# Kernel tuning notes

Measured on AMD Instinct MI355X. Metric: run time of the kernel, lower is better.

The kernel has to match this reference:

```python
import jax, jax.numpy as jnp
import numpy as np

N_HEAD = 16
ROPE_BASE = 10000.0


def _rope_tables(T, head_dim, dtype):
    inv_freq = 1.0 / (ROPE_BASE ** (jnp.arange(0, head_dim, 2, dtype=jnp.float32) / head_dim))
    t = jnp.arange(T, dtype=jnp.float32)
    freqs = t[:, None] * inv_freq[None, :]          # [T, hd/2]
    emb = jnp.concatenate([freqs, freqs], axis=-1)  # [T, hd]
    return jnp.cos(emb).astype(dtype), jnp.sin(emb).astype(dtype)


def _rotate_half(x):
    h = x.shape[-1] // 2
    return jnp.concatenate([-x[..., h:], x[..., :h]], axis=-1)


def setup_inputs() -> dict:
    key = jax.random.key(0)
    k1, k2, k3 = jax.random.split(key, 3)
    B, T, C = 2, 2048, 1024
    x = jax.random.normal(k1, (B, T, C), dtype=jnp.float32)
    w_attn = jax.random.normal(k2, (3 * C, C), dtype=jnp.float32) * (1.0 / np.sqrt(C))
    w_proj = jax.random.normal(k3, (C, C), dtype=jnp.float32) * (1.0 / np.sqrt(C))
    return {"x": x, "w_attn": w_attn, "w_proj": w_proj}


def reference(x, w_attn, w_proj):
    B, T, C = x.shape
    H = N_HEAD
    hd = C // H

    qkv = jnp.einsum('btc,fc->btf', x, w_attn)          # [B,T,3C]
    q, k, v = jnp.split(qkv, 3, axis=-1)
    # [B,H,T,hd]
    q = q.reshape(B, T, H, hd).transpose(0, 2, 1, 3)
    k = k.reshape(B, T, H, hd).transpose(0, 2, 1, 3)
    v = v.reshape(B, T, H, hd).transpose(0, 2, 1, 3)

    cos, sin = _rope_tables(T, hd, x.dtype)             # [T,hd]
    cos = cos[None, None]
    sin = sin[None, None]
    q = q * cos + _rotate_half(q) * sin
    k = k * cos + _rotate_half(k) * sin

    scale = 1.0 / np.sqrt(hd)
    scores = jnp.einsum('bhqd,bhkd->bhqk', q, k) * scale  # [B,H,T,T]
    causal = jnp.tril(jnp.ones((T, T), dtype=bool))
    scores = jnp.where(causal[None, None], scores, jnp.finfo(scores.dtype).min)
    attn = jax.nn.softmax(scores, axis=-1)
    out = jnp.einsum('bhqk,bhkd->bhqd', attn, v)          # [B,H,T,hd]
    out = out.transpose(0, 2, 1, 3).reshape(B, T, C)
    return jnp.einsum('btc,oc->bto', out, w_proj)
```

## Files before the change

kernel.cpp:

```cpp
#include <hip/hip_runtime.h>
#include <hip/hip_bf16.h>
#include <stdint.h>

typedef unsigned short u16;
typedef __bf16 bf16x8 __attribute__((ext_vector_type(8)));
typedef float f32x4 __attribute__((ext_vector_type(4)));

#define B_ 2
#define T_ 2048
#define C_ 1024
#define H_ 16
#define HD 64
#define M_ (B_ * T_)
#define N3 (3 * C_)

__device__ __forceinline__ float bf2f(u16 u) {
  return __uint_as_float(((unsigned int)u) << 16);
}
__device__ __forceinline__ u16 f2bf(float f) {
  unsigned int u = __float_as_uint(f);
  u += 0x7FFF + ((u >> 16) & 1);
  return (u16)(u >> 16);
}
__device__ __forceinline__ unsigned cvt_pk_bf16(float lo, float hi) {
  unsigned r;
  asm("v_cvt_pk_bf16_f32 %0, %1, %2" : "=v"(r) : "v"(lo), "v"(hi));
  return r;
}
__device__ __forceinline__ void async16(void* ldsp, const void* gp) {
  __builtin_amdgcn_global_load_lds(
      (const __attribute__((address_space(1))) unsigned int*)gp,
      (__attribute__((address_space(3))) unsigned int*)ldsp, 16, 0, 0);
}

union U16x8 { uint4 v; u16 u[8]; };

__device__ __forceinline__ bf16x8 ldsAfrag(const char* base, int row, int kbyte) {
  int off = (row * 128 + kbyte) ^ ((row & 7) << 4);
  uint4 t = *reinterpret_cast<const uint4*>(base + off);
  return __builtin_bit_cast(bf16x8, t);
}
__device__ __forceinline__ bf16x8 ldsRead(const char* p) {
  uint4 t = *reinterpret_cast<const uint4*>(p);
  return __builtin_bit_cast(bf16x8, t);
}

__global__ void cvt_bf16(const float* __restrict__ src, u16* __restrict__ dst, int n4) {
  int i = blockIdx.x * blockDim.x + threadIdx.x;
  int stride = gridDim.x * blockDim.x;
  for (; i < n4; i += stride) {
    float4 v = reinterpret_cast<const float4*>(src)[i];
    uint2 o;
    o.x = (unsigned)f2bf(v.x) | ((unsigned)f2bf(v.y) << 16);
    o.y = (unsigned)f2bf(v.z) | ((unsigned)f2bf(v.w) << 16);
    reinterpret_cast<uint2*>(dst)[i] = o;
  }
}

__global__ void rope_tables_kernel(float* __restrict__ cosT, float* __restrict__ sinT) {
  int t = blockIdx.x;
  int i = threadIdx.x;
  float inv = powf(10000.0f, -(float)i * (1.0f / 32.0f));
  float f = (float)t * inv;
  cosT[t * 32 + i] = cosf(f);
  sinT[t * 32 + i] = sinf(f);
}

template <bool OUT_F32>
__global__ __launch_bounds__(256) void gemm_bt(const u16* __restrict__ A,
                                               const u16* __restrict__ Bw,
                                               void* __restrict__ Cout,
                                               int M, int N, int K) {
  __shared__ uint4 ldsbuf[2048];
  char* As = (char*)ldsbuf;
  char* Bs = (char*)ldsbuf + 16384;
  const int tid = threadIdx.x;
  const int lane = tid & 63;
  const int wv = tid >> 6;
  const int wr = wv >> 1, wc = wv & 1;
  const int lrow = lane & 15, lgrp = lane >> 4;
  const long m0 = (long)blockIdx.x * 128, n0 = (long)blockIdx.y * 128;
  const int srow_l = lane >> 3;
  const int csrc = ((lane & 7) ^ (lane >> 3)) * 8;
  f32x4 acc[4][4] = {};
  for (int k0 = 0; k0 < K; k0 += 64) {
    __syncthreads();
#pragma unroll
    for (int p = 0; p < 4; ++p) {
      int seg = wv * 4 + p;
      int row = seg * 8 + srow_l;
      async16(As + seg * 1024, A + (size_t)(m0 + row) * K + k0 + csrc);
      async16(Bs + seg * 1024, Bw + (size_t)(n0 + row) * K + k0 + csrc);
    }
    __syncthreads();
#pragma unroll
    for (int ks = 0; ks < 2; ++ks) {
      bf16x8 af[4], bfr[4];
#pragma unroll
      for (int i = 0; i < 4; ++i) {
        af[i]  = ldsAfrag(As, wr * 64 + i * 16 + lrow, ks * 64 + lgrp * 16);
        bfr[i] = ldsAfrag(Bs, wc * 64 + i * 16 + lrow, ks * 64 + lgrp * 16);
      }
#pragma unroll
      for (int i = 0; i < 4; ++i)
#pragma unroll
        for (int j = 0; j < 4; ++j)
          acc[i][j] = __builtin_amdgcn_mfma_f32_16x16x32_bf16(af[i], bfr[j], acc[i][j], 0, 0, 0);
    }
  }
#pragma unroll
  for (int i = 0; i < 4; ++i)
#pragma unroll
    for (int j = 0; j < 4; ++j) {
      long r0 = m0 + wr * 64 + i * 16 + lgrp * 4;
      long c  = n0 + wc * 64 + j * 16 + lrow;
#pragma unroll
      for (int r = 0; r < 4; ++r) {
        float v = acc[i][j][r];
        if (OUT_F32)
          ((float*)Cout)[(r0 + r) * N + c] = v;
        else
          ((u16*)Cout)[(r0 + r) * N + c] = f2bf(v);
      }
    }
}

__global__ __launch_bounds__(256) void rope_reshape(const u16* __restrict__ qkv,
                                                    const float* __restrict__ cosT,
                                                    const float* __restrict__ sinT,
                                                    u16* __restrict__ Q,
                                                    u16* __restrict__ K,
                                                    u16* __restrict__ Vt) {
  __shared__ u16 Vs[64][80];
  const float SCLQ = 0.125f * 1.4426950408889634f;
  const int tid = threadIdx.x;
  const int tblk = blockIdx.x, bh = blockIdx.y;
  const int b = bh >> 4, h = bh & 15;
  const int tl = tid >> 2, quar = tid & 3;
  const int t = tblk * 64 + tl;
  const u16* rowp = qkv + ((size_t)(b * T_ + t)) * N3 + h * HD;
  const int d0 = quar * 8;
  float cs[8], sn[8];
#pragma unroll
  for (int j = 0; j < 8; ++j) {
    cs[j] = cosT[t * 32 + d0 + j];
    sn[j] = sinT[t * 32 + d0 + j];
  }
#pragma unroll
  for (int part = 0; part < 2; ++part) {
    const u16* p = rowp + part * C_;
    U16x8 x1, x2, o1, o2;
    x1.v = *reinterpret_cast<const uint4*>(p + d0);
    x2.v = *reinterpret_cast<const uint4*>(p + d0 + 32);
#pragma unroll
    for (int j = 0; j < 8; ++j) {
      float a = bf2f(x1.u[j]), c2 = bf2f(x2.u[j]);
      float f1 = a * cs[j] - c2 * sn[j];
      float f2 = c2 * cs[j] + a * sn[j];
      if (part == 0) { f1 *= SCLQ; f2 *= SCLQ; }
      o1.u[j] = f2bf(f1);
      o2.u[j] = f2bf(f2);
    }
    u16* dst = (part ? K : Q) + ((size_t)bh * T_ + t) * HD;
    *reinterpret_cast<uint4*>(dst + d0) = o1.v;
    *reinterpret_cast<uint4*>(dst + d0 + 32) = o2.v;
  }
  const u16* pv = rowp + 2 * C_;
#pragma unroll
  for (int c = 0; c < 2; ++c) {
    int d = quar * 16 + c * 8;
    *reinterpret_cast<uint4*>(&Vs[tl][d]) = *reinterpret_cast<const uint4*>(pv + d);
  }
  __syncthreads();
  const int d = tid >> 2, tq = tid & 3;
  U16x8 a, bv;
#pragma unroll
  for (int j = 0; j < 8; ++j) a.u[j] = Vs[tq * 16 + j][d];
#pragma unroll
  for (int j = 0; j < 8; ++j) bv.u[j] = Vs[tq * 16 + 8 + j][d];
  u16* dstv = Vt + ((size_t)bh * HD + d) * T_ + tblk * 64 + tq * 16;
  *reinterpret_cast<uint4*>(dstv) = a.v;
  *reinterpret_cast<uint4*>(dstv + 8) = bv.v;
}

__global__ __launch_bounds__(256) void attn_fwd11(const u16* __restrict__ Q,
                                                  const u16* __restrict__ K,
                                                  const u16* __restrict__ Vt,
                                                  u16* __restrict__ O) {
  __shared__ uint4 lds4[2560];
  char* ldsb = (char*)lds4;
  const int tid = threadIdx.x;
  const int lane = tid & 63, wv = tid >> 6;
  const int lrow = lane & 15, lgrp = lane >> 4;
  const int bh = blockIdx.y;
  const int b = bh >> 4, h = bh & 15;
  const u16* Qh = Q + (size_t)bh * T_ * HD;
  const u16* Kh = K + (size_t)bh * T_ * HD;
  const u16* Vh = Vt + (size_t)bh * HD * T_;

  const int srow_l = lane >> 3;
  const int csrc = ((lane & 7) ^ (lane >> 3)) * 8;

  auto stage = [&](int slot, int kt) {
    char* Kd = ldsb + (slot << 14);
    char* Vd = Kd + 8192;
    const u16* Kg = Kh + (size_t)(kt * 64) * HD;
    const u16* Vg = Vh + kt * 64;
#pragma unroll
    for (int seg = 0; seg < 2; ++seg) {
      int row = wv * 16 + seg * 8 + srow_l;
      async16(Kd + wv * 2048 + seg * 1024, Kg + (size_t)row * HD + csrc);
      async16(Vd + wv * 2048 + seg * 1024, Vg + (size_t)row * T_ + csrc);
    }
  };

  const int swz = (lrow & 7) << 4;
  const int krA = lrow * 128 + ((lgrp * 16) ^ swz);
  const int krB = lrow * 128 + ((64 + lgrp * 16) ^ swz);
  const int vrA = 8192 + krA;
  const int vrB = 8192 + krB;
  char* PsW = ldsb + 32768 + wv * 2048 + lrow * 128;
  char* pw0 = PsW + ((0 * 32 + lgrp * 8) ^ swz);
  char* pw1 = PsW + ((1 * 32 + lgrp * 8) ^ swz);
  char* pw2 = PsW + ((2 * 32 + lgrp * 8) ^ swz);
  char* pw3 = PsW + ((3 * 32 + lgrp * 8) ^ swz);
  const char* paA = PsW + ((lgrp * 16) ^ swz);
  const char* paB = PsW + ((64 + lgrp * 16) ^ swz);

  uint4 ones4;
  ones4.x = ones4.y = ones4.z = ones4.w = 0x3F803F80u;
  const bf16x8 ones8 = __builtin_bit_cast(bf16x8, ones4);

  const int unit = 31 - (int)blockIdx.x;
  const int qs = unit * 64;
  const int q_glob = qs + wv * 16 + lrow;
  const int nu = unit + 1;

  bf16x8 qf[2];
#pragma unroll
  for (int ks = 0; ks < 2; ++ks) {
    uint4 t4 = *reinterpret_cast<const uint4*>(
        Qh + (size_t)(qs + wv * 16 + lrow) * HD + ks * 32 + lgrp * 8);
    qf[ks] = __builtin_bit_cast(bf16x8, t4);
  }
  f32x4 o[4] = {};
  f32x4 lacc = {};

  stage(0, 0);
  __syncthreads();

  int cur = 0;
  for (int kt = 0; kt < nu; ++kt) {
    if (kt + 1 < nu) stage(cur ^ 1, kt + 1);
    const char* buf = ldsb + (cur << 14);
    const char* KbA = buf + krA;
    const char* KbB = buf + krB;
    const char* VbA = buf + vrA;
    const char* VbB = buf + vrB;

    f32x4 s[4] = {};
    __builtin_amdgcn_s_setprio(1);
#pragma unroll
    for (int n = 0; n < 4; ++n)
      s[n] = __builtin_amdgcn_mfma_f32_16x16x32_bf16(ldsRead(KbA + n * 2048), qf[0], s[n], 0, 0, 0);
#pragma unroll
    for (int n = 0; n < 4; ++n)
      s[n] = __builtin_amdgcn_mfma_f32_16x16x32_bf16(ldsRead(KbB + n * 2048), qf[1], s[n], 0, 0, 0);
    __builtin_amdgcn_s_setprio(0);

    if (kt == nu - 1) {
#pragma unroll
      for (int n = 0; n < 4; ++n)
#pragma unroll
        for (int r = 0; r < 4; ++r) {
          int kg = kt * 64 + n * 16 + lgrp * 4 + r;
          float v = (kg <= q_glob) ? s[n][r] : -__builtin_inff();
          s[n][r] = exp2f(v);
        }
    } else {
#pragma unroll
      for (int n = 0; n < 4; ++n)
#pragma unroll
        for (int r = 0; r < 4; ++r) s[n][r] = exp2f(s[n][r]);
    }

    {
      uint2 w0, w1, w2, w3;
      w0.x = cvt_pk_bf16(s[0][0], s[0][1]); w0.y = cvt_pk_bf16(s[0][2], s[0][3]);
      w1.x = cvt_pk_bf16(s[1][0], s[1][1]); w1.y = cvt_pk_bf16(s[1][2], s[1][3]);
      w2.x = cvt_pk_bf16(s[2][0], s[2][1]); w2.y = cvt_pk_bf16(s[2][2], s[2][3]);
      w3.x = cvt_pk_bf16(s[3][0], s[3][1]); w3.y = cvt_pk_bf16(s[3][2], s[3][3]);
      *reinterpret_cast<uint2*>(pw0) = w0;
      *reinterpret_cast<uint2*>(pw1) = w1;
      *reinterpret_cast<uint2*>(pw2) = w2;
      *reinterpret_cast<uint2*>(pw3) = w3;
    }

    __builtin_amdgcn_s_setprio(1);
#pragma unroll
    for (int ks = 0; ks < 2; ++ks) {
      bf16x8 pa = ldsRead(ks ? paB : paA);
      lacc = __builtin_amdgcn_mfma_f32_16x16x32_bf16(pa, ones8, lacc, 0, 0, 0);
      const char* vbb = ks ? VbB : VbA;
#pragma unroll
      for (int dn = 0; dn < 4; ++dn) {
        bf16x8 bv = ldsRead(vbb + dn * 2048);
        o[dn] = __builtin_amdgcn_mfma_f32_16x16x32_bf16(pa, bv, o[dn], 0, 0, 0);
      }
    }
    __builtin_amdgcn_s_setprio(0);
    __syncthreads();
    cur ^= 1;
  }

#pragma unroll
  for (int r = 0; r < 4; ++r) {
    float inv = 1.0f / lacc[r];
    int t = qs + wv * 16 + lgrp * 4 + r;
#pragma unroll
    for (int dn = 0; dn < 4; ++dn) {
      int c = h * HD + dn * 16 + lrow;
      O[((size_t)(b * T_ + t)) * C_ + c] = f2bf(o[dn][r] * inv);
    }
  }
}

extern "C" void kernel_launch(void* const* d_in, const int* in_sizes, int n_in,
                              void* d_out, int out_size, void* d_ws, size_t ws_size,
                              hipStream_t stream) {
  const float* x  = (const float*)d_in[0];
  const float* wa = (const float*)d_in[1];
  const float* wp = (const float*)d_in[2];
  float* out = (float*)d_out;
  char* ws = (char*)d_ws;
  size_t off = 0;
  auto alloc = [&](size_t bytes) {
    char* p = ws + off;
    off += (bytes + 255) & ~(size_t)255;
    return p;
  };
  u16* xb   = (u16*)alloc((size_t)M_ * C_ * 2);
  u16* wab  = (u16*)alloc((size_t)N3 * C_ * 2);
  u16* wpb  = (u16*)alloc((size_t)C_ * C_ * 2);
  u16* qkvb = (u16*)alloc((size_t)M_ * N3 * 2);
  u16* Qb   = (u16*)alloc((size_t)B_ * H_ * T_ * HD * 2);
  u16* Kb   = (u16*)alloc((size_t)B_ * H_ * T_ * HD * 2);
  u16* Vtb  = (u16*)alloc((size_t)B_ * H_ * T_ * HD * 2);
  u16* Ob   = (u16*)alloc((size_t)M_ * C_ * 2);
  float* cosT = (float*)alloc((size_t)T_ * 32 * 4);
  float* sinT = (float*)alloc((size_t)T_ * 32 * 4);
  (void)in_sizes; (void)n_in; (void)out_size; (void)ws_size;

  cvt_bf16<<<1024, 256, 0, stream>>>(x, xb, M_ * C_ / 4);
  cvt_bf16<<<1024, 256, 0, stream>>>(wa, wab, N3 * C_ / 4);
  cvt_bf16<<<512, 256, 0, stream>>>(wp, wpb, C_ * C_ / 4);
  rope_tables_kernel<<<T_, 32, 0, stream>>>(cosT, sinT);
  gemm_bt<false><<<dim3(M_ / 128, N3 / 128), 256, 0, stream>>>(xb, wab, qkvb, M_, N3, C_);
  rope_reshape<<<dim3(T_ / 64, B_ * H_), 256, 0, stream>>>(qkvb, cosT, sinT, Qb, Kb, Vtb);
  attn_fwd11<<<dim3(32, B_ * H_), 256, 0, stream>>>(Qb, Kb, Vtb, Ob);
  gemm_bt<true><<<dim3(M_ / 128, C_ / 128), 256, 0, stream>>>(Ob, wpb, out, M_, C_, C_);
}
```

Baseline: 139.8 us.

## Process 128 query rows per attention block to reuse K/V tiles

The attention kernel now gives each wave two 16-row query tiles, so a block covers 128 queries instead of 64. Each K and V fragment read from LDS feeds two MFMAs, halving K/V staging traffic per query. The cost is a grid of 512 blocks instead of 1024, more registers per thread and a larger P buffer in LDS, which may lower occupancy. Because the grid is half as large, causal load imbalance across CUs is coarser.

```diff
diff --git a/kernel.cpp b/kernel.cpp
--- a/kernel.cpp
+++ b/kernel.cpp
@@ -183,11 +183,11 @@
   *reinterpret_cast<uint4*>(dstv + 8) = bv.v;
 }
 
-__global__ __launch_bounds__(256) void attn_fwd11(const u16* __restrict__ Q,
+__global__ __launch_bounds__(256) void attn_fwd12(const u16* __restrict__ Q,
                                                   const u16* __restrict__ K,
                                                   const u16* __restrict__ Vt,
                                                   u16* __restrict__ O) {
-  __shared__ uint4 lds4[2560];
+  __shared__ uint4 lds4[3072];
   char* ldsb = (char*)lds4;
   const int tid = threadIdx.x;
   const int lane = tid & 63, wv = tid >> 6;
@@ -219,7 +219,7 @@
   const int krB = lrow * 128 + ((64 + lgrp * 16) ^ swz);
   const int vrA = 8192 + krA;
   const int vrB = 8192 + krB;
-  char* PsW = ldsb + 32768 + wv * 2048 + lrow * 128;
+  char* PsW = ldsb + 32768 + wv * 4096 + lrow * 128;
   char* pw0 = PsW + ((0 * 32 + lgrp * 8) ^ swz);
   char* pw1 = PsW + ((1 * 32 + lgrp * 8) ^ swz);
   char* pw2 = PsW + ((2 * 32 + lgrp * 8) ^ swz);
@@ -231,20 +231,23 @@
   ones4.x = ones4.y = ones4.z = ones4.w = 0x3F803F80u;
   const bf16x8 ones8 = __builtin_bit_cast(bf16x8, ones4);
 
-  const int unit = 31 - (int)blockIdx.x;
-  const int qs = unit * 64;
-  const int q_glob = qs + wv * 16 + lrow;
-  const int nu = unit + 1;
-
-  bf16x8 qf[2];
-#pragma unroll
-  for (int ks = 0; ks < 2; ++ks) {
-    uint4 t4 = *reinterpret_cast<const uint4*>(
-        Qh + (size_t)(qs + wv * 16 + lrow) * HD + ks * 32 + lgrp * 8);
-    qf[ks] = __builtin_bit_cast(bf16x8, t4);
-  }
-  f32x4 o[4] = {};
-  f32x4 lacc = {};
+  const int unit = 15 - (int)blockIdx.x;
+  const int q0 = unit * 128;
+  const int qg0 = q0 + wv * 32 + lrow;
+  const int qg1 = qg0 + 16;
+  const int nu = unit * 2 + 2;
+
+  bf16x8 qf[2][2];
+#pragma unroll
+  for (int m = 0; m < 2; ++m)
+#pragma unroll
+    for (int ks = 0; ks < 2; ++ks) {
+      uint4 t4 = *reinterpret_cast<const uint4*>(
+          Qh + (size_t)(q0 + wv * 32 + m * 16 + lrow) * HD + ks * 32 + lgrp * 8);
+      qf[m][ks] = __builtin_bit_cast(bf16x8, t4);
+    }
+  f32x4 o[2][4] = {};
+  f32x4 lacc[2] = {};
 
   stage(0, 0);
   __syncthreads();
@@ -258,54 +261,68 @@
     const char* VbA = buf + vrA;
     const char* VbB = buf + vrB;
 
-    f32x4 s[4] = {};
+    f32x4 s[2][4] = {};
     __builtin_amdgcn_s_setprio(1);
 #pragma unroll
-    for (int n = 0; n < 4; ++n)
-      s[n] = __builtin_amdgcn_mfma_f32_16x16x32_bf16(ldsRead(KbA + n * 2048), qf[0], s[n], 0, 0, 0);
-#pragma unroll
-    for (int n = 0; n < 4; ++n)
-      s[n] = __builtin_amdgcn_mfma_f32_16x16x32_bf16(ldsRead(KbB + n * 2048), qf[1], s[n], 0, 0, 0);
+    for (int n = 0; n < 4; ++n) {
+      bf16x8 bk = ldsRead(KbA + n * 2048);
+      s[0][n] = __builtin_amdgcn_mfma_f32_16x16x32_bf16(bk, qf[0][0], s[0][n], 0, 0, 0);
+      s[1][n] = __builtin_amdgcn_mfma_f32_16x16x32_bf16(bk, qf[1][0], s[1][n], 0, 0, 0);
+    }
+#pragma unroll
+    for (int n = 0; n < 4; ++n) {
+      bf16x8 bk = ldsRead(KbB + n * 2048);
+      s[0][n] = __builtin_amdgcn_mfma_f32_16x16x32_bf16(bk, qf[0][1], s[0][n], 0, 0, 0);
+      s[1][n] = __builtin_amdgcn_mfma_f32_16x16x32_bf16(bk, qf[1][1], s[1][n], 0, 0, 0);
+    }
     __builtin_amdgcn_s_setprio(0);
 
-    if (kt == nu - 1) {
+    if (kt >= nu - 2) {
 #pragma unroll
       for (int n = 0; n < 4; ++n)
 #pragma unroll
         for (int r = 0; r < 4; ++r) {
           int kg = kt * 64 + n * 16 + lgrp * 4 + r;
-          float v = (kg <= q_glob) ? s[n][r] : -__builtin_inff();
-          s[n][r] = exp2f(v);
+          s[0][n][r] = exp2f((kg <= qg0) ? s[0][n][r] : -__builtin_inff());
+          s[1][n][r] = exp2f((kg <= qg1) ? s[1][n][r] : -__builtin_inff());
         }
     } else {
 #pragma unroll
       for (int n = 0; n < 4; ++n)
 #pragma unroll
-        for (int r = 0; r < 4; ++r) s[n][r] = exp2f(s[n][r]);
-    }
-
-    {
+        for (int r = 0; r < 4; ++r) {
+          s[0][n][r] = exp2f(s[0][n][r]);
+          s[1][n][r] = exp2f(s[1][n][r]);
+        }
+    }
+
+#pragma unroll
+    for (int m = 0; m < 2; ++m) {
       uint2 w0, w1, w2, w3;
-      w0.x = cvt_pk_bf16(s[0][0], s[0][1]); w0.y = cvt_pk_bf16(s[0][2], s[0][3]);
-      w1.x = cvt_pk_bf16(s[1][0], s[1][1]); w1.y = cvt_pk_bf16(s[1][2], s[1][3]);
-      w2.x = cvt_pk_bf16(s[2][0], s[2][1]); w2.y = cvt_pk_bf16(s[2][2], s[2][3]);
-      w3.x = cvt_pk_bf16(s[3][0], s[3][1]); w3.y = cvt_pk_bf16(s[3][2], s[3][3]);
-      *reinterpret_cast<uint2*>(pw0) = w0;
-      *reinterpret_cast<uint2*>(pw1) = w1;
-      *reinterpret_cast<uint2*>(pw2) = w2;
-      *reinterpret_cast<uint2*>(pw3) = w3;
+      w0.x = cvt_pk_bf16(s[m][0][0], s[m][0][1]); w0.y = cvt_pk_bf16(s[m][0][2], s[m][0][3]);
+      w1.x = cvt_pk_bf16(s[m][1][0], s[m][1][1]); w1.y = cvt_pk_bf16(s[m][1][2], s[m][1][3]);
+      w2.x = cvt_pk_bf16(s[m][2][0], s[m][2][1]); w2.y = cvt_pk_bf16(s[m][2][2], s[m][2][3]);
+      w3.x = cvt_pk_bf16(s[m][3][0], s[m][3][1]); w3.y = cvt_pk_bf16(s[m][3][2], s[m][3][3]);
+      *reinterpret_cast<uint2*>(pw0 + m * 2048) = w0;
+      *reinterpret_cast<uint2*>(pw1 + m * 2048) = w1;
+      *reinterpret_cast<uint2*>(pw2 + m * 2048) = w2;
+      *reinterpret_cast<uint2*>(pw3 + m * 2048) = w3;
     }
 
     __builtin_amdgcn_s_setprio(1);
 #pragma unroll
     for (int ks = 0; ks < 2; ++ks) {
-      bf16x8 pa = ldsRead(ks ? paB : paA);
-      lacc = __builtin_amdgcn_mfma_f32_16x16x32_bf16(pa, ones8, lacc, 0, 0, 0);
+      const char* pab = ks ? paB : paA;
+      bf16x8 pa0 = ldsRead(pab);
+      bf16x8 pa1 = ldsRead(pab + 2048);
+      lacc[0] = __builtin_amdgcn_mfma_f32_16x16x32_bf16(pa0, ones8, lacc[0], 0, 0, 0);
+      lacc[1] = __builtin_amdgcn_mfma_f32_16x16x32_bf16(pa1, ones8, lacc[1], 0, 0, 0);
       const char* vbb = ks ? VbB : VbA;
 #pragma unroll
       for (int dn = 0; dn < 4; ++dn) {
         bf16x8 bv = ldsRead(vbb + dn * 2048);
-        o[dn] = __builtin_amdgcn_mfma_f32_16x16x32_bf16(pa, bv, o[dn], 0, 0, 0);
+        o[0][dn] = __builtin_amdgcn_mfma_f32_16x16x32_bf16(pa0, bv, o[0][dn], 0, 0, 0);
+        o[1][dn] = __builtin_amdgcn_mfma_f32_16x16x32_bf16(pa1, bv, o[1][dn], 0, 0, 0);
       }
     }
     __builtin_amdgcn_s_setprio(0);
@@ -314,15 +331,17 @@
   }
 
 #pragma unroll
-  for (int r = 0; r < 4; ++r) {
-    float inv = 1.0f / lacc[r];
-    int t = qs + wv * 16 + lgrp * 4 + r;
-#pragma unroll
-    for (int dn = 0; dn < 4; ++dn) {
-      int c = h * HD + dn * 16 + lrow;
-      O[((size_t)(b * T_ + t)) * C_ + c] = f2bf(o[dn][r] * inv);
-    }
-  }
+  for (int m = 0; m < 2; ++m)
+#pragma unroll
+    for (int r = 0; r < 4; ++r) {
+      float inv = 1.0f / lacc[m][r];
+      int t = q0 + wv * 32 + m * 16 + lgrp * 4 + r;
+#pragma unroll
+      for (int dn = 0; dn < 4; ++dn) {
+        int c = h * HD + dn * 16 + lrow;
+        O[((size_t)(b * T_ + t)) * C_ + c] = f2bf(o[m][dn][r] * inv);
+      }
+    }
 }
 
 extern "C" void kernel_launch(void* const* d_in, const int* in_sizes, int n_in,
@@ -357,6 +376,6 @@
   rope_tables_kernel<<<T_, 32, 0, stream>>>(cosT, sinT);
   gemm_bt<false><<<dim3(M_ / 128, N3 / 128), 256, 0, stream>>>(xb, wab, qkvb, M_, N3, C_);
   rope_reshape<<<dim3(T_ / 64, B_ * H_), 256, 0, stream>>>(qkvb, cosT, sinT, Qb, Kb, Vtb);
-  attn_fwd11<<<dim3(32, B_ * H_), 256, 0, stream>>>(Qb, Kb, Vtb, Ob);
+  attn_fwd12<<<dim3(16, B_ * H_), 256, 0, stream>>>(Qb, Kb, Vtb, Ob);
   gemm_bt<true><<<dim3(M_ / 128, C_ / 128), 256, 0, stream>>>(Ob, wpb, out, M_, C_, C_);
 }
```

Result: slower. 145.4 us (+4.0%).
